# Kernel optimization log

Hardware: AMD Instinct MI355X
Metric: run time of the kernel (lower is better)

## Reference

```python
import jax, jax.numpy as jnp
import numpy as np

# ---- problem constants (match init_kwargs) ----
LAM = 1.0; MU = 1.0; D0 = 1.0; NMIN = 1.0; NMAX = 99; ALPHA = 2.0
BATCH = 2048; N_STEPS = 64; T = 1.0; HIDDEN = 128


def _U(x):
    return D0 / (x + NMIN) ** ALPHA


def _delta_n(pre_n, dt, forward, k, rng):
    # faithful numpy port of PolymerDiffusion.delta_N (jump sizes shared across batch per call)
    log_res = -np.log(rng.random(k))
    lsk = np.concatenate([[0.0], np.cumsum(log_res / LAM / 2)])
    msk = np.concatenate([[0.0], np.cumsum(log_res / MU / 2)])
    jl = int(np.searchsorted(lsk[1:], dt, side='right'))  # first j with dt < lsk[j+1]
    jm = int(np.searchsorted(msk[1:], dt, side='right'))
    if jl >= k: jl = 0  # no break -> delta stays 0
    if jm >= k: jm = 0
    eta = rng.random(pre_n.shape[0])
    if forward:
        d_up = np.where(pre_n <= NMAX - jl, jl, 0)
        d_dn = np.where(pre_n >= jm, -jm, 0)
    else:
        d_up = np.where(pre_n >= jl, jl, 0)
        d_dn = np.where(pre_n <= NMAX - jm, -jm, 0)
    return np.where(eta < 0.5, d_up, d_dn).astype(np.float64)


def _get_samples(dt, N, rng):
    B = BATCH
    X1 = np.zeros((B, N + 1)); X1[:, 0] = rng.integers(0, NMAX + 1, B)
    X2 = np.zeros((B, N + 1))
    dB = rng.standard_normal((B, N)) * np.sqrt(dt)
    for i in range(N):
        X1[:, i + 1] = X1[:, i] + _delta_n(X1[:, i], dt, True, 5, rng)
        X2[:, i + 1] = X2[:, i] + _U(X1[:, i]) * dt + dB[:, i]
    X1b = rng.integers(0, NMAX + 1, (B, N + 1)).astype(np.float64)
    X2b = np.zeros((B, N + 1))
    dBb = rng.standard_normal((B, N)) * np.sqrt(dt)
    X1b[:, N] = X1[:, N]; X2b[:, N] = X2[:, N]
    for i in range(N):
        X1b[:, N - i - 1] = X1b[:, N - i] - _delta_n(X1b[:, N - i], dt, False, 5, rng)
        X2b[:, N - i - 1] = X2b[:, N - i] - _U(X1b[:, N - i]) * dt - dBb[:, N - i - 1]
    return (np.concatenate([X1, X1b], 0), np.concatenate([X2, X2b], 0), np.concatenate([dB, dBb], 0))


def setup_inputs() -> dict:
    rng = np.random.default_rng(0)
    dt = T / N_STEPS
    n_np, s_np, dB_np = _get_samples(dt, N_STEPS, rng)
    key = jax.random.key(0)
    ks = jax.random.split(key, 4)
    def w(k, fi, fo):
        return jax.random.normal(k, (fi, fo), jnp.float32) / np.sqrt(fi).astype(np.float32)
    return {
        'W1': w(ks[0], 2, HIDDEN), 'b1': jnp.zeros(HIDDEN, jnp.float32),
        'W2': w(ks[1], HIDDEN, HIDDEN), 'b2': jnp.zeros(HIDDEN, jnp.float32),
        'W3': w(ks[2], HIDDEN, HIDDEN), 'b3': jnp.zeros(HIDDEN, jnp.float32),
        'W4': w(ks[3], HIDDEN, NMAX + 1), 'b4': jnp.zeros(NMAX + 1, jnp.float32),
        'samples_n': jnp.asarray(n_np, jnp.int32),      # [2B, N+1]
        'samples_s': jnp.asarray(s_np, jnp.float32),    # [2B, N+1]
        'samples_deltaB': jnp.asarray(dB_np, jnp.float32),  # [2B, N]
        't': jnp.float32(T),
    }


def reference(W1, b1, W2, b2, W3, b3, W4, b4, samples_n, samples_s, samples_deltaB, t):
    N = samples_deltaB.shape[1]
    dt = t / N
    out_dim = W4.shape[1]  # nmax + 1

    def u_scalar(s, tk, n):
        x = jnp.stack([s, tk])  # [2]
        h = jnp.tanh(x @ W1 + b1)
        h = jnp.tanh(h @ W2 + b2)
        h = jnp.tanh(h @ W3 + b3)
        return (h @ W4 + b4)[n]

    du = jax.grad(u_scalar, 0)
    ddu = jax.grad(du, 0)
    u_v = jax.vmap(u_scalar)
    du_v = jax.vmap(du)
    ddu_v = jax.vmap(ddu)

    B2 = samples_s.shape[0]
    tk0 = jnp.broadcast_to(t, (B2,))
    sN, nN = samples_s[:, N], samples_n[:, N]
    u = u_v(sN, tk0, nN)
    ps = du_v(sN, tk0, nN)
    pss = ddu_v(sN, tk0, nN)

    # step i uses column N-1-i and time tk = t - i*dt (tk decremented AFTER get_partial, as in source)
    dB_rev = samples_deltaB[:, ::-1].T            # [N, 2B]
    s_rev = samples_s[:, N - 1::-1].T             # [N, 2B]
    n_rev = samples_n[:, N - 1::-1].T             # [N, 2B]
    tks = t - dt * jnp.arange(N, dtype=samples_s.dtype)  # [N]

    def step(carry, xs):
        u, ps, pss = carry
        dB, s_col, n_col, tk = xs
        u = u - ps * dB - pss * dt * 0.5
        tkv = jnp.broadcast_to(tk, s_col.shape)
        ps = du_v(s_col, tkv, n_col)
        pss = ddu_v(s_col, tkv, n_col)
        return (u, ps, pss), None

    (u, _, _), _ = jax.lax.scan(step, (u, ps, pss), (dB_rev, s_rev, n_rev, tks))

    beta = 1e6
    s0 = samples_s[:, 0]
    u0 = jnp.sqrt(beta / (2 * jnp.pi)) * jnp.exp(-beta * s0 ** 2 / 2) / out_dim
    return (u[:, None], u0[:, None])
```

## Files before the change

kernel.cpp:

```cpp
#include <hip/hip_runtime.h>
#include <hip/hip_fp16.h>
#include <math.h>

#define HIDDEN 128
#define NSTEP  64
#define BATCH2 4096
#define OUTD   100

typedef __attribute__((ext_vector_type(4))) _Float16 f16x4;
typedef __attribute__((ext_vector_type(8))) _Float16 f16x8;
typedef __attribute__((ext_vector_type(4))) float    f32x4;

static __device__ __forceinline__ f32x4 mfma16(f16x4 a, f16x4 b, f32x4 c) {
    return __builtin_amdgcn_mfma_f32_16x16x16f16(a, b, c, 0, 0, 0);
}
static __device__ __forceinline__ unsigned h2u(__half2 h) {
    return __builtin_bit_cast(unsigned, h);
}
static __device__ __forceinline__ __half2 u2h(unsigned u) {
    return __builtin_bit_cast(__half2, u);
}
static __device__ __forceinline__ f16x4 frag2(__half2 lo, __half2 hi) {
    uint2 p = { h2u(lo), h2u(hi) };
    return __builtin_bit_cast(f16x4, p);
}

static __device__ __forceinline__ void tanh_chain_h2(
    __half2 z, __half2 zd, __half2 zdd,
    __half2& a, __half2& ad, __half2& add)
{
    const __half2 one = __float2half2_rn(1.0f);
    const __half2 two = __float2half2_rn(2.0f);
    __half2 e = h2exp(__hadd2(z, z));
    __half2 w = __hmul2(two, h2rcp(__hadd2(e, one)));
    a  = __hsub2(one, w);
    __half2 g = __hmul2(w, __hsub2(two, w));
    ad = __hmul2(g, zd);
    __half2 p = __hmul2(a, zd);
    __half2 u = __hadd2(p, p);
    add = __hsub2(__hmul2(g, zdd), __hmul2(u, ad));
}

__global__ __launch_bounds__(256) void setup_kernel(
    const float* __restrict__ W2, const float* __restrict__ W3,
    const float* __restrict__ W4,
    const float* __restrict__ samples_s,
    __half* __restrict__ wbf, float* __restrict__ out)
{
    int t = blockIdx.x * blockDim.x + threadIdx.x;
    int m = t >> 14, r = t & 16383, n = r >> 7, k = r & 127;
    const float* W = m ? W3 : W2;
    wbf[t] = __float2half(W[k * HIDDEN + n]);
    if (t < OUTD * HIDDEN) {
        int nn = t >> 7, h = t & 127;
        wbf[32768 + t] = __float2half(W4[h * OUTD + nn]);
    }
    if (t < BATCH2) {
        out[t] = 0.0f;
        float s0 = samples_s[t * (NSTEP + 1)];
        out[BATCH2 + t] = 3.9894228040143267f * expf(-500000.0f * s0 * s0);
    }
}

__global__ __launch_bounds__(256, 3) void eval_kernel(
    const float* __restrict__ W1, const float* __restrict__ b1,
    const float* __restrict__ b2, const float* __restrict__ b3,
    const float* __restrict__ b4,
    const __half* __restrict__ wbf,
    const int*   __restrict__ samples_n,
    const float* __restrict__ samples_s,
    const float* __restrict__ samples_dB,
    const float* __restrict__ tptr,
    float* __restrict__ out)
{
    __shared__ short ldsW[HIDDEN * HIDDEN];
    __shared__ float ldsB2[HIDDEN];
    __shared__ float ldsB3[HIDDEN];

    const int tid  = threadIdx.x;
    const int w    = tid >> 6;
    const int lane = tid & 63;
    const int m16  = lane & 15;
    const int q    = lane >> 4;
    const int b    = blockIdx.x;

    const int k0    = 2 * lane;
    const int pBase = ((k0 >> 2) & 3) * 32 + (k0 >> 4) * 4 + (k0 & 3);

    if (tid < HIDDEN) {
        ldsB2[tid] = b2[tid];
        ldsB3[tid] = b3[tid];
    }
    #pragma unroll 4
    for (int it = 0; it < 32; ++it) {
        int r = w * 32 + it;
        unsigned val = *(const unsigned*)((const short*)wbf + r * 128 + k0);
        *(unsigned*)(ldsW + r * 128 + ((pBase + 8 * (r & 15)) & 127)) = val;
    }

    const float t  = tptr[0];
    const float dt = t / (float)NSTEP;
    const int   j  = 16 * w + m16;
    const int   c  = NSTEP - j;
    const float s  = samples_s[b * (NSTEP + 1) + c];
    const int   n  = samples_n[b * (NSTEP + 1) + c];
    const float dB = samples_dB[b * NSTEP + (NSTEP - 1 - j)];
    const float tk = (j == 0) ? t : t - dt * (float)(j - 1);

    f16x4 Bv[8], Bd[8], Bdd[8];
    const __half2 zero2 = __float2half2_rn(0.0f);
    #pragma unroll
    for (int kt = 0; kt < 8; ++kt) {
        const int h0 = 16 * kt + 4 * q;
        float4 wa = *(const float4*)(W1 + h0);
        float4 wb = *(const float4*)(W1 + HIDDEN + h0);
        float4 bb = *(const float4*)(b1 + h0);
        __half2 z0 = __floats2half2_rn(fmaf(wa.x, s, fmaf(wb.x, tk, bb.x)),
                                       fmaf(wa.y, s, fmaf(wb.y, tk, bb.y)));
        __half2 z1 = __floats2half2_rn(fmaf(wa.z, s, fmaf(wb.z, tk, bb.z)),
                                       fmaf(wa.w, s, fmaf(wb.w, tk, bb.w)));
        __half2 zd0 = __floats2half2_rn(wa.x, wa.y);
        __half2 zd1 = __floats2half2_rn(wa.z, wa.w);
        __half2 a0, ad0, add0, a1, ad1, add1;
        tanh_chain_h2(z0, zd0, zero2, a0, ad0, add0);
        tanh_chain_h2(z1, zd1, zero2, a1, ad1, add1);
        Bv[kt]  = frag2(a0,  a1);
        Bd[kt]  = frag2(ad0, ad1);
        Bdd[kt] = frag2(add0, add1);
    }

    __syncthreads();

    f16x4 Nv[8], Nd[8], Ndd[8];
    #pragma unroll
    for (int mt = 0; mt < 8; ++mt) {
        const short* lw = ldsW + (16 * mt + m16) * 128;
        f32x4 aV = {0.f,0.f,0.f,0.f}, aD = {0.f,0.f,0.f,0.f}, aDD = {0.f,0.f,0.f,0.f};
        #pragma unroll
        for (int kp = 0; kp < 4; ++kp) {
            int off = (q * 32 + kp * 8 + 8 * m16) & 127;
            f16x8 aw = *(const f16x8*)(lw + off);
            f16x4 alo = (f16x4){aw[0], aw[1], aw[2], aw[3]};
            f16x4 ahi = (f16x4){aw[4], aw[5], aw[6], aw[7]};
            aV  = mfma16(alo, Bv [2*kp], aV );
            aD  = mfma16(alo, Bd [2*kp], aD );
            aDD = mfma16(alo, Bdd[2*kp], aDD);
            aV  = mfma16(ahi, Bv [2*kp+1], aV );
            aD  = mfma16(ahi, Bd [2*kp+1], aD );
            aDD = mfma16(ahi, Bdd[2*kp+1], aDD);
        }
        const int h0 = 16 * mt + 4 * q;
        float4 bias = *(const float4*)(ldsB2 + h0);
        __half2 a0, ad0, add0, a1, ad1, add1;
        tanh_chain_h2(__floats2half2_rn(aV[0] + bias.x, aV[1] + bias.y),
                      __floats2half2_rn(aD[0], aD[1]),
                      __floats2half2_rn(aDD[0], aDD[1]), a0, ad0, add0);
        tanh_chain_h2(__floats2half2_rn(aV[2] + bias.z, aV[3] + bias.w),
                      __floats2half2_rn(aD[2], aD[3]),
                      __floats2half2_rn(aDD[2], aDD[3]), a1, ad1, add1);
        Nv[mt]  = frag2(a0,  a1);
        Nd[mt]  = frag2(ad0, ad1);
        Ndd[mt] = frag2(add0, add1);
    }

    __syncthreads();

    #pragma unroll 4
    for (int it = 0; it < 32; ++it) {
        int r = w * 32 + it;
        unsigned val = *(const unsigned*)((const short*)wbf + HIDDEN * HIDDEN + r * 128 + k0);
        *(unsigned*)(ldsW + r * 128 + ((pBase + 8 * (r & 15)) & 127)) = val;
    }
    __syncthreads();

    const __half* __restrict__ w4t = wbf + 2 * HIDDEN * HIDDEN;
    __half2 accV = zero2, accD = zero2, accDD = zero2;
    #pragma unroll
    for (int mt = 0; mt < 8; ++mt) {
        const short* lw = ldsW + (16 * mt + m16) * 128;
        f32x4 aV = {0.f,0.f,0.f,0.f}, aD = {0.f,0.f,0.f,0.f}, aDD = {0.f,0.f,0.f,0.f};
        #pragma unroll
        for (int kp = 0; kp < 4; ++kp) {
            int off = (q * 32 + kp * 8 + 8 * m16) & 127;
            f16x8 aw = *(const f16x8*)(lw + off);
            f16x4 alo = (f16x4){aw[0], aw[1], aw[2], aw[3]};
            f16x4 ahi = (f16x4){aw[4], aw[5], aw[6], aw[7]};
            aV  = mfma16(alo, Nv [2*kp], aV );
            aD  = mfma16(alo, Nd [2*kp], aD );
            aDD = mfma16(alo, Ndd[2*kp], aDD);
            aV  = mfma16(ahi, Nv [2*kp+1], aV );
            aD  = mfma16(ahi, Nd [2*kp+1], aD );
            aDD = mfma16(ahi, Ndd[2*kp+1], aDD);
        }
        const int h0 = 16 * mt + 4 * q;
        float4 bias = *(const float4*)(ldsB3 + h0);
        uint2 w4u = *(const uint2*)(w4t + n * HIDDEN + h0);
        __half2 w4lo = u2h(w4u.x), w4hi = u2h(w4u.y);
        __half2 a0, ad0, add0, a1, ad1, add1;
        tanh_chain_h2(__floats2half2_rn(aV[0] + bias.x, aV[1] + bias.y),
                      __floats2half2_rn(aD[0], aD[1]),
                      __floats2half2_rn(aDD[0], aDD[1]), a0, ad0, add0);
        tanh_chain_h2(__floats2half2_rn(aV[2] + bias.z, aV[3] + bias.w),
                      __floats2half2_rn(aD[2], aD[3]),
                      __floats2half2_rn(aDD[2], aDD[3]), a1, ad1, add1);
        accV  = __hfma2(a0,  w4lo, accV );  accV  = __hfma2(a1,  w4hi, accV );
        accD  = __hfma2(ad0, w4lo, accD );  accD  = __hfma2(ad1, w4hi, accD );
        accDD = __hfma2(add0, w4lo, accDD); accDD = __hfma2(add1, w4hi, accDD);
    }
    float sv  = __low2float(accV)  + __high2float(accV);
    float sd  = __low2float(accD)  + __high2float(accD);
    float sdd = __low2float(accDD) + __high2float(accDD);

    sd  += __shfl_xor(sd,  16, 64);  sd  += __shfl_xor(sd,  32, 64);
    sdd += __shfl_xor(sdd, 16, 64);  sdd += __shfl_xor(sdd, 32, 64);
    sv  += __shfl_xor(sv,  16, 64);  sv  += __shfl_xor(sv,  32, 64);

    float contrib = -(sd * dB + sdd * dt * 0.5f);
    if (j == 0) contrib += sv + b4[n];

    contrib += __shfl_xor(contrib, 1, 64);
    contrib += __shfl_xor(contrib, 2, 64);
    contrib += __shfl_xor(contrib, 4, 64);
    contrib += __shfl_xor(contrib, 8, 64);
    if (lane == 0) atomicAdd(&out[b], contrib);
}

extern "C" void kernel_launch(void* const* d_in, const int* in_sizes, int n_in,
                              void* d_out, int out_size, void* d_ws, size_t ws_size,
                              hipStream_t stream) {
    const float* W1 = (const float*)d_in[0];
    const float* b1 = (const float*)d_in[1];
    const float* W2 = (const float*)d_in[2];
    const float* b2 = (const float*)d_in[3];
    const float* W3 = (const float*)d_in[4];
    const float* b3 = (const float*)d_in[5];
    const float* W4 = (const float*)d_in[6];
    const float* b4 = (const float*)d_in[7];
    const int*   sn  = (const int*)d_in[8];
    const float* ss  = (const float*)d_in[9];
    const float* sdB = (const float*)d_in[10];
    const float* t   = (const float*)d_in[11];
    float* out = (float*)d_out;
    __half* wbf = (__half*)d_ws;

    setup_kernel<<<(2 * HIDDEN * HIDDEN) / 256, 256, 0, stream>>>(W2, W3, W4, ss, wbf, out);
    eval_kernel<<<BATCH2, 256, 0, stream>>>(
        W1, b1, b2, b3, b4, wbf, sn, ss, sdB, t, out);
}
```

Before: 165.4 us.

## Pre-swizzle weights into MFMA fragment order and load via global_load_lds

The setup kernel now writes W2/W3 in half precision already arranged in the per-lane MFMA A-fragment order. The eval kernel can then copy each weight matrix into LDS with 16-byte direct global-to-LDS loads instead of 4-byte register round-trips with swizzled stores. The LDS reads become contiguous per-lane 16-byte accesses with simpler addressing. This depends on global_load_lds behaving correctly with the barrier and on the layout remap being exactly right.

Measured after the change: 160.4 us. 3.0% less time.

```diff
diff --git a/kernel.cpp b/kernel.cpp
--- a/kernel.cpp
+++ b/kernel.cpp
@@ -23,6 +23,12 @@
 static __device__ __forceinline__ f16x4 frag2(__half2 lo, __half2 hi) {
     uint2 p = { h2u(lo), h2u(hi) };
     return __builtin_bit_cast(f16x4, p);
+}
+
+static __device__ __forceinline__ void load_lds16(const void* g, void* l) {
+    __builtin_amdgcn_global_load_lds(
+        (const __attribute__((address_space(1))) void*)g,
+        (__attribute__((address_space(3))) void*)l, 16, 0, 0);
 }
 
 static __device__ __forceinline__ void tanh_chain_h2(
@@ -48,9 +54,16 @@
     __half* __restrict__ wbf, float* __restrict__ out)
 {
     int t = blockIdx.x * blockDim.x + threadIdx.x;
-    int m = t >> 14, r = t & 16383, n = r >> 7, k = r & 127;
-    const float* W = m ? W3 : W2;
-    wbf[t] = __float2half(W[k * HIDDEN + n]);
+    int l   = t >> 14;
+    int pos = t & 16383;
+    int chunk = pos >> 9;
+    int mt = chunk >> 2, kp = chunk & 3;
+    int lane = (pos >> 3) & 63;
+    int i = pos & 7;
+    int row = 16 * mt + (lane & 15);
+    int k   = 32 * kp + 16 * (i >> 2) + 4 * (lane >> 4) + (i & 3);
+    const float* W = l ? W3 : W2;
+    wbf[t] = __float2half(W[k * HIDDEN + row]);
     if (t < OUTD * HIDDEN) {
         int nn = t >> 7, h = t & 127;
         wbf[32768 + t] = __float2half(W4[h * OUTD + nn]);
@@ -73,7 +86,7 @@
     const float* __restrict__ tptr,
     float* __restrict__ out)
 {
-    __shared__ short ldsW[HIDDEN * HIDDEN];
+    __shared__ __align__(16) short ldsW[HIDDEN * HIDDEN];
     __shared__ float ldsB2[HIDDEN];
     __shared__ float ldsB3[HIDDEN];
 
@@ -84,18 +97,17 @@
     const int q    = lane >> 4;
     const int b    = blockIdx.x;
 
-    const int k0    = 2 * lane;
-    const int pBase = ((k0 >> 2) & 3) * 32 + (k0 >> 4) * 4 + (k0 & 3);
-
     if (tid < HIDDEN) {
         ldsB2[tid] = b2[tid];
         ldsB3[tid] = b3[tid];
     }
-    #pragma unroll 4
-    for (int it = 0; it < 32; ++it) {
-        int r = w * 32 + it;
-        unsigned val = *(const unsigned*)((const short*)wbf + r * 128 + k0);
-        *(unsigned*)(ldsW + r * 128 + ((pBase + 8 * (r & 15)) & 127)) = val;
+    {
+        const short* g2 = (const short*)wbf;
+        #pragma unroll
+        for (int it = 0; it < 8; ++it) {
+            int idx = w * 8 + it;
+            load_lds16(g2 + idx * 512 + lane * 8, ldsW + idx * 512);
+        }
     }
 
     const float t  = tptr[0];
@@ -134,12 +146,10 @@
     f16x4 Nv[8], Nd[8], Ndd[8];
     #pragma unroll
     for (int mt = 0; mt < 8; ++mt) {
-        const short* lw = ldsW + (16 * mt + m16) * 128;
         f32x4 aV = {0.f,0.f,0.f,0.f}, aD = {0.f,0.f,0.f,0.f}, aDD = {0.f,0.f,0.f,0.f};
         #pragma unroll
         for (int kp = 0; kp < 4; ++kp) {
-            int off = (q * 32 + kp * 8 + 8 * m16) & 127;
-            f16x8 aw = *(const f16x8*)(lw + off);
+            f16x8 aw = *(const f16x8*)(ldsW + ((mt * 4 + kp) << 9) + (lane << 3));
             f16x4 alo = (f16x4){aw[0], aw[1], aw[2], aw[3]};
             f16x4 ahi = (f16x4){aw[4], aw[5], aw[6], aw[7]};
             aV  = mfma16(alo, Bv [2*kp], aV );
@@ -165,11 +175,13 @@
 
     __syncthreads();
 
-    #pragma unroll 4
-    for (int it = 0; it < 32; ++it) {
-        int r = w * 32 + it;
-        unsigned val = *(const unsigned*)((const short*)wbf + HIDDEN * HIDDEN + r * 128 + k0);
-        *(unsigned*)(ldsW + r * 128 + ((pBase + 8 * (r & 15)) & 127)) = val;
+    {
+        const short* g3 = (const short*)(wbf + HIDDEN * HIDDEN);
+        #pragma unroll
+        for (int it = 0; it < 8; ++it) {
+            int idx = w * 8 + it;
+            load_lds16(g3 + idx * 512 + lane * 8, ldsW + idx * 512);
+        }
     }
     __syncthreads();
 
@@ -177,12 +189,10 @@
     __half2 accV = zero2, accD = zero2, accDD = zero2;
     #pragma unroll
     for (int mt = 0; mt < 8; ++mt) {
-        const short* lw = ldsW + (16 * mt + m16) * 128;
         f32x4 aV = {0.f,0.f,0.f,0.f}, aD = {0.f,0.f,0.f,0.f}, aDD = {0.f,0.f,0.f,0.f};
         #pragma unroll
         for (int kp = 0; kp < 4; ++kp) {
-            int off = (q * 32 + kp * 8 + 8 * m16) & 127;
-            f16x8 aw = *(const f16x8*)(lw + off);
+            f16x8 aw = *(const f16x8*)(ldsW + ((mt * 4 + kp) << 9) + (lane << 3));
             f16x4 alo = (f16x4){aw[0], aw[1], aw[2], aw[3]};
             f16x4 ahi = (f16x4){aw[4], aw[5], aw[6], aw[7]};
             aV  = mfma16(alo, Nv [2*kp], aV );
```
